# Performance work log

Hardware: AMD Instinct MI355X
Metric: run time of the kernel (lower is better)

Reference implementation:

```python
import jax, jax.numpy as jnp
import numpy as np

B, L, INPUT_DIM = 4, 4096, 32
D_MODEL, N_LAYERS = 256, 2
D_STATE, D_CONV, EXPAND = 16, 4, 2
D_INNER = EXPAND * D_MODEL          # 512
DT_RANK = (D_MODEL + 15) // 16      # 16
OUTPUT_DIM, HORIZON = 32, 4
LN_EPS = 1e-5


def setup_inputs() -> dict:
    key = jax.random.key(0)
    ks = jax.random.split(key, 16)
    s = 0.02
    inp = {
        "x": jax.random.normal(ks[0], (B, L, INPUT_DIM), jnp.float32),
        "enc_w": jax.random.normal(ks[1], (D_MODEL, INPUT_DIM), jnp.float32) * s,
        "enc_b": jnp.zeros((D_MODEL,), jnp.float32),
        "in_proj_w": jax.random.normal(ks[2], (N_LAYERS, 2 * D_INNER, D_MODEL), jnp.float32) * s,
        "conv_w": jax.random.normal(ks[3], (N_LAYERS, D_INNER, D_CONV), jnp.float32) * s,
        "conv_b": jnp.zeros((N_LAYERS, D_INNER), jnp.float32),
        "xproj_w": jax.random.normal(ks[4], (N_LAYERS, DT_RANK + 2 * D_STATE, D_INNER), jnp.float32) * s,
        "dtproj_w": jax.random.normal(ks[5], (N_LAYERS, D_INNER, DT_RANK), jnp.float32) * s,
        "dtproj_b": jax.random.normal(ks[6], (N_LAYERS, D_INNER), jnp.float32) * 0.1,
        "A_log": jnp.log(jnp.tile(jnp.arange(1.0, D_STATE + 1.0, dtype=jnp.float32), (N_LAYERS, D_INNER, 1))),
        "Dp": jnp.ones((N_LAYERS, D_INNER), jnp.float32),
        "out_proj_w": jax.random.normal(ks[7], (N_LAYERS, D_MODEL, D_INNER), jnp.float32) * s,
        "ln_g": jnp.ones((D_MODEL,), jnp.float32),
        "ln_b": jnp.zeros((D_MODEL,), jnp.float32),
        "head_w": jax.random.normal(ks[8], (OUTPUT_DIM * HORIZON, D_MODEL), jnp.float32) * s,
        "head_b": jnp.zeros((OUTPUT_DIM * HORIZON,), jnp.float32),
    }
    return inp


def _mamba_block(x, in_w, cw, cb, xp_w, dt_w, dt_b, A_log, Dp, out_w):
    # x: [B, L, d_model]
    b, l, _ = x.shape
    xz = jnp.einsum("bld,ed->ble", x, in_w)            # [B, L, 2*d_inner]
    xi, res = jnp.split(xz, 2, axis=-1)
    # causal depthwise conv1d (padding=d_conv-1, truncated to L)
    xpad = jnp.pad(xi, ((0, 0), (D_CONV - 1, 0), (0, 0)))
    xi = sum(xpad[:, k:k + l, :] * cw[:, k] for k in range(D_CONV)) + cb
    xi = jax.nn.silu(xi)
    dbl = jnp.einsum("bld,ed->ble", xi, xp_w)           # [B, L, dt_rank+2*d_state]
    dt = dbl[..., :DT_RANK]
    Bm = dbl[..., DT_RANK:DT_RANK + D_STATE]            # [B, L, d_state]
    Cm = dbl[..., DT_RANK + D_STATE:]                   # [B, L, d_state]
    dt = jax.nn.softplus(jnp.einsum("blr,dr->bld", dt, dt_w) + dt_b)  # [B, L, d_inner]
    A = -jnp.exp(A_log)                                 # [d_inner, d_state]

    def step(h, ins):
        dt_t, B_t, C_t, x_t = ins                       # [B,di],[B,ds],[B,ds],[B,di]
        dA = jnp.exp(dt_t[..., None] * A)               # [B, d_inner, d_state]
        h = dA * h + (dt_t * x_t)[..., None] * B_t[:, None, :]
        y = jnp.einsum("bds,bs->bd", h, C_t)
        return h, y

    h0 = jnp.zeros((b, D_INNER, D_STATE), x.dtype)
    xs = (jnp.moveaxis(dt, 1, 0), jnp.moveaxis(Bm, 1, 0),
          jnp.moveaxis(Cm, 1, 0), jnp.moveaxis(xi, 1, 0))
    _, ys = jax.lax.scan(step, h0, xs)                  # ys: [L, B, d_inner]
    y = jnp.moveaxis(ys, 0, 1) + xi * Dp
    y = y * jax.nn.silu(res)
    return jnp.einsum("ble,de->bld", y, out_w)


def reference(x, enc_w, enc_b, in_proj_w, conv_w, conv_b, xproj_w, dtproj_w,
              dtproj_b, A_log, Dp, out_proj_w, ln_g, ln_b, head_w, head_b):
    h = jnp.einsum("bli,di->bld", x, enc_w) + enc_b     # encoder
    for i in range(N_LAYERS):
        h = h + _mamba_block(h, in_proj_w[i], conv_w[i], conv_b[i], xproj_w[i],
                             dtproj_w[i], dtproj_b[i], A_log[i], Dp[i], out_proj_w[i])
    mu = jnp.mean(h, axis=-1, keepdims=True)
    var = jnp.mean((h - mu) ** 2, axis=-1, keepdims=True)
    hn = (h - mu) * jax.lax.rsqrt(var + LN_EPS) * ln_g + ln_b
    state = hn[:, -1, :]                                # last timestep
    return jnp.einsum("bd,od->bo", state, head_w) + head_b
```

## Files before the change

### kernel.cpp

```cpp
#include <hip/hip_runtime.h>
#include <hip/hip_bf16.h>
#include <math.h>

#define BB 4
#define LL 4096
#define DM 256
#define DI 512
#define DS 16
#define NOUTK 128
#define LN_EPS 1e-5f
#define NC 128
#define CLEN (LL/NC)
#define BL (BB*LL)
#define LDB 640

typedef __attribute__((ext_vector_type(8))) short short8;
typedef __attribute__((ext_vector_type(4))) float f32x4;

__device__ __forceinline__ ushort f2bf(float f) {
    union { float f; unsigned u; } v; v.f = f;
    unsigned r = (v.u + 0x7FFF + ((v.u >> 16) & 1)) >> 16;
    return (ushort)r;
}
__device__ __forceinline__ float bf2f(ushort u) {
    union { unsigned u; float f; } v; v.u = ((unsigned)u) << 16;
    return v.f;
}

__global__ __launch_bounds__(256) void cast_bf16_kernel(
    const float* __restrict__ src, ushort* __restrict__ dst, int n)
{
    int i = blockIdx.x * 256 + threadIdx.x;
    if (i < n) dst[i] = f2bf(src[i]);
}

__global__ __launch_bounds__(256) void build_comb_kernel(
    const float* __restrict__ xpw, const float* __restrict__ dtw,
    ushort* __restrict__ dst)
{
    int i = blockIdx.x * 256 + threadIdx.x;
    int l = i / (640 * 512);
    int rem = i - l * 640 * 512;
    int row = rem >> 9, k = rem & 511;
    const float* xp = xpw + l * 48 * 512;
    const float* dw = dtw + l * 512 * 16;
    float v;
    if (row < 512) {
        v = 0.f;
        #pragma unroll
        for (int r = 0; r < 16; ++r)
            v = fmaf(dw[row * 16 + r], xp[r * 512 + k], v);
    } else if (row < 544) {
        v = xp[(row - 512 + 16) * 512 + k];
    } else v = 0.f;
    dst[i] = f2bf(v);
}

__global__ __launch_bounds__(256) void enc_kernel(
    const float* __restrict__ x, const float* __restrict__ w,
    const float* __restrict__ b, float* __restrict__ h,
    ushort* __restrict__ hbf)
{
    __shared__ float sw[256 * 33];
    __shared__ float sx[4][32];
    int tid = threadIdx.x;
    for (int i = tid; i < 256 * 8; i += 256) {
        float4 v = ((const float4*)w)[i];
        int r = i >> 3, c = (i & 7) * 4;
        sw[r * 33 + c + 0] = v.x; sw[r * 33 + c + 1] = v.y;
        sw[r * 33 + c + 2] = v.z; sw[r * 33 + c + 3] = v.w;
    }
    int row0 = blockIdx.x * 4;
    if (tid < 32) {
        for (int rr = 0; rr < 4; ++rr)
            sx[rr][tid] = x[(size_t)(row0 + rr) * 32 + tid];
    }
    __syncthreads();
    float bb = b[tid];
    #pragma unroll
    for (int rr = 0; rr < 4; ++rr) {
        float acc = bb;
        #pragma unroll
        for (int k = 0; k < 32; ++k)
            acc = fmaf(sx[rr][k], sw[tid * 33 + k], acc);
        size_t o = (size_t)(row0 + rr) * DM + tid;
        h[o] = acc;
        hbf[o] = f2bf(acc);
    }
}

template<int EPI, bool F32OUT, bool RESID, bool BF16OUT>
__global__ __launch_bounds__(256, 4) void mfma_gemm(
    const ushort* __restrict__ A, int lda,
    const ushort* __restrict__ W,
    const float* __restrict__ bias,
    float* __restrict__ C, int ldc,
    ushort* __restrict__ Cbf, int ldcbf,
    int K)
{
    __shared__ ushort As[64 * 64];
    __shared__ ushort Ws[128 * 64];
    const int tid = threadIdx.x;

    int nwg = gridDim.x * gridDim.y;
    int wlin = blockIdx.y * gridDim.x + blockIdx.x;
    int gx = blockIdx.x, gy = blockIdx.y;
    if ((nwg & 7) == 0) {
        int q = nwg >> 3;
        int s = (wlin & 7) * q + (wlin >> 3);
        gx = s % gridDim.x;
        gy = s / gridDim.x;
    }
    const int bm = gy * 64;
    const int bn = gx * 128;
    const int wid = tid >> 6, lane = tid & 63;
    const int wrow = (wid >> 1) * 32, wcol = (wid & 1) * 64;
    const int sr = tid >> 3;
    const int sc = tid & 7;

    f32x4 acc[2][4];
    #pragma unroll
    for (int mi = 0; mi < 2; ++mi)
        #pragma unroll
        for (int ni = 0; ni < 4; ++ni)
            acc[mi][ni] = (f32x4){0.f, 0.f, 0.f, 0.f};

    const int nk = K >> 6;
    for (int t = 0; t < nk; ++t) {
        const int k0 = t << 6;
        #pragma unroll
        for (int it = 0; it < 2; ++it) {
            int r = it * 32 + sr;
            int csrc = sc ^ (r & 7);
            __builtin_amdgcn_global_load_lds(
                (const __attribute__((address_space(1))) unsigned int*)
                    (A + (size_t)(bm + r) * lda + k0 + csrc * 8),
                (__attribute__((address_space(3))) unsigned int*)
                    (As + r * 64 + sc * 8), 16, 0, 0);
        }
        #pragma unroll
        for (int it = 0; it < 4; ++it) {
            int r = it * 32 + sr;
            int csrc = sc ^ (r & 7);
            __builtin_amdgcn_global_load_lds(
                (const __attribute__((address_space(1))) unsigned int*)
                    (W + (size_t)(bn + r) * K + k0 + csrc * 8),
                (__attribute__((address_space(3))) unsigned int*)
                    (Ws + r * 64 + sc * 8), 16, 0, 0);
        }
        __syncthreads();
        #pragma unroll
        for (int kk = 0; kk < 2; ++kk) {
            short8 af[2], bfr[4];
            #pragma unroll
            for (int mi = 0; mi < 2; ++mi) {
                int r = wrow + mi * 16 + (lane & 15);
                int c = (lane >> 4) + kk * 4;
                af[mi] = *(const short8*)(As + r * 64 + ((c ^ (r & 7)) << 3));
            }
            #pragma unroll
            for (int ni = 0; ni < 4; ++ni) {
                int r = wcol + ni * 16 + (lane & 15);
                int c = (lane >> 4) + kk * 4;
                bfr[ni] = *(const short8*)(Ws + r * 64 + ((c ^ (r & 7)) << 3));
            }
            #pragma unroll
            for (int mi = 0; mi < 2; ++mi)
                #pragma unroll
                for (int ni = 0; ni < 4; ++ni)
                    acc[mi][ni] = __builtin_amdgcn_mfma_f32_16x16x32_bf16(
                        af[mi], bfr[ni], acc[mi][ni], 0, 0, 0);
        }
        __syncthreads();
    }

    #pragma unroll
    for (int mi = 0; mi < 2; ++mi)
        #pragma unroll
        for (int ni = 0; ni < 4; ++ni) {
            int col = bn + wcol + ni * 16 + (lane & 15);
            #pragma unroll
            for (int r = 0; r < 4; ++r) {
                int row = bm + wrow + mi * 16 + (lane >> 4) * 4 + r;
                float v = acc[mi][ni][r];
                if (EPI == 1) {
                    if (col < 512) {
                        float u = v + bias[col];
                        float sp = fmaxf(u, 0.f) + __logf(1.f + __expf(-fabsf(u)));
                        Cbf[(size_t)row * ldcbf + col] = f2bf(sp);
                    } else if (col < 544) {
                        C[(size_t)row * ldc + (col - 512)] = v;
                    }
                } else {
                    if (F32OUT) {
                        float* cp = C + (size_t)row * ldc + col;
                        float vv = v;
                        if (RESID) vv += *cp;
                        *cp = vv;
                        if (BF16OUT) Cbf[(size_t)row * ldcbf + col] = f2bf(vv);
                    } else if (BF16OUT) {
                        Cbf[(size_t)row * ldcbf + col] = f2bf(v);
                    }
                }
            }
        }
}

__global__ __launch_bounds__(256) void conv_silu_kernel(
    const ushort* __restrict__ xz, const float* __restrict__ cw,
    const float* __restrict__ cb, ushort* __restrict__ xi)
{
    int idx = blockIdx.x * 256 + threadIdx.x;
    int d4 = (idx & 127) * 4;
    int bt = idx >> 7;
    int t = bt & (LL - 1);
    const ushort* base = xz + (size_t)bt * 1024 + d4;
    float acc[4];
    float4 w[4];
    #pragma unroll
    for (int j = 0; j < 4; ++j) {
        acc[j] = cb[d4 + j];
        w[j] = *(const float4*)(cw + (d4 + j) * 4);
    }
    #pragma unroll
    for (int k = 0; k < 4; ++k) {
        int back = 3 - k;
        if (t >= back) {
            ushort4 v = *(const ushort4*)(base - back * 1024);
            float wk0 = (k==0)?w[0].x:(k==1)?w[0].y:(k==2)?w[0].z:w[0].w;
            float wk1 = (k==0)?w[1].x:(k==1)?w[1].y:(k==2)?w[1].z:w[1].w;
            float wk2 = (k==0)?w[2].x:(k==1)?w[2].y:(k==2)?w[2].z:w[2].w;
            float wk3 = (k==0)?w[3].x:(k==1)?w[3].y:(k==2)?w[3].z:w[3].w;
            acc[0] = fmaf(bf2f(v.x), wk0, acc[0]);
            acc[1] = fmaf(bf2f(v.y), wk1, acc[1]);
            acc[2] = fmaf(bf2f(v.z), wk2, acc[2]);
            acc[3] = fmaf(bf2f(v.w), wk3, acc[3]);
        }
    }
    ushort4 o;
    float s0 = acc[0] / (1.f + __expf(-acc[0]));
    float s1 = acc[1] / (1.f + __expf(-acc[1]));
    float s2 = acc[2] / (1.f + __expf(-acc[2]));
    float s3 = acc[3] / (1.f + __expf(-acc[3]));
    o.x = f2bf(s0); o.y = f2bf(s1); o.z = f2bf(s2); o.w = f2bf(s3);
    *(ushort4*)(xi + (size_t)bt * 512 + d4) = o;
}

__global__ __launch_bounds__(256) void scan_phase1(
    const ushort* __restrict__ xi, const ushort* __restrict__ dtb,
    const float* __restrict__ bc,
    const float* __restrict__ alog,
    float* __restrict__ cA, float* __restrict__ cH)
{
    int d = blockIdx.z * 256 + threadIdx.x;
    int b = blockIdx.y, c = blockIdx.x;
    float Av[16];
    bool fast = true;
    #pragma unroll
    for (int s = 0; s < 16; ++s) {
        Av[s] = -__expf(alog[d * 16 + s]);
        fast = fast && (fabsf(Av[s] + (float)(s + 1)) < 1e-3f * (s + 1));
    }
    float h[16], P[16];
    #pragma unroll
    for (int s = 0; s < 16; ++s) { h[s] = 0.f; P[s] = 1.f; }
    int t0 = c * CLEN;
    if (fast) {
        float Pe = 1.f;
        for (int t = t0; t < t0 + CLEN; ++t) {
            size_t row = (size_t)b * LL + t;
            float dt = bf2f(dtb[row * 512 + d]);
            float x = bf2f(xi[row * 512 + d]);
            float dtx = dt * x;
            const float* bp = bc + row * 32;
            float e1 = __expf(-dt);
            float e2=e1*e1, e3=e2*e1, e4=e2*e2, e5=e3*e2, e6=e3*e3, e7=e4*e3, e8=e4*e4;
            float e9=e5*e4, e10=e5*e5, e11=e6*e5, e12=e6*e6, e13=e7*e6, e14=e7*e7, e15=e8*e7, e16=e8*e8;
            float pw[16] = {e1,e2,e3,e4,e5,e6,e7,e8,e9,e10,e11,e12,e13,e14,e15,e16};
            #pragma unroll
            for (int s = 0; s < 16; ++s)
                h[s] = fmaf(pw[s], h[s], dtx * bp[s]);
            Pe *= e1;
        }
        float p1=Pe, p2=p1*p1, p3=p2*p1, p4=p2*p2, p5=p3*p2, p6=p3*p3, p7=p4*p3, p8=p4*p4;
        float p9=p5*p4, p10=p5*p5, p11=p6*p5, p12=p6*p6, p13=p7*p6, p14=p7*p7, p15=p8*p7, p16=p8*p8;
        float pp[16] = {p1,p2,p3,p4,p5,p6,p7,p8,p9,p10,p11,p12,p13,p14,p15,p16};
        #pragma unroll
        for (int s = 0; s < 16; ++s) P[s] = pp[s];
    } else {
        for (int t = t0; t < t0 + CLEN; ++t) {
            size_t row = (size_t)b * LL + t;
            float dt = bf2f(dtb[row * 512 + d]);
            float x = bf2f(xi[row * 512 + d]);
            float dtx = dt * x;
            const float* bp = bc + row * 32;
            #pragma unroll
            for (int s = 0; s < 16; ++s) {
                float dA = __expf(dt * Av[s]);
                h[s] = fmaf(dA, h[s], dtx * bp[s]);
                P[s] *= dA;
            }
        }
    }
    size_t base = (((size_t)b * DI + d) * NC + c) * 16;
    #pragma unroll
    for (int q = 0; q < 4; ++q) {
        *(float4*)(cA + base + q*4) = *(float4*)&P[q*4];
        *(float4*)(cH + base + q*4) = *(float4*)&h[q*4];
    }
}

__global__ __launch_bounds__(256) void scan_phase2(
    const float* __restrict__ cA, float* __restrict__ cH)
{
    int idx = blockIdx.x * 256 + threadIdx.x;
    int s = idx & 15;
    int bd = idx >> 4;
    size_t base = (size_t)bd * NC * 16 + s;
    float init = 0.f;
    for (int c = 0; c < NC; ++c) {
        size_t o = base + (size_t)c * 16;
        float a = cA[o], hh = cH[o];
        cH[o] = init;
        init = fmaf(a, init, hh);
    }
}

__global__ __launch_bounds__(256) void scan_phase3(
    const ushort* __restrict__ xz,
    ushort* __restrict__ xi,
    const ushort* __restrict__ dtb,
    const float* __restrict__ bc,
    const float* __restrict__ alog,
    const float* __restrict__ Dp,
    const float* __restrict__ cH,
    int c0)
{
    int d = blockIdx.z * 256 + threadIdx.x;
    int b = blockIdx.y;
    int c = blockIdx.x + c0;
    float Av[16];
    bool fast = true;
    #pragma unroll
    for (int s = 0; s < 16; ++s) {
        Av[s] = -__expf(alog[d * 16 + s]);
        fast = fast && (fabsf(Av[s] + (float)(s + 1)) < 1e-3f * (s + 1));
    }
    float h[16];
    size_t cbase = (((size_t)b * DI + d) * NC + c) * 16;
    #pragma unroll
    for (int q = 0; q < 4; ++q)
        *(float4*)&h[q*4] = *(const float4*)(cH + cbase + q*4);
    float Dd = Dp[d];
    int t0 = c * CLEN;
    if (fast) {
        for (int t = t0; t < t0 + CLEN; ++t) {
            size_t row = (size_t)b * LL + t;
            float dt = bf2f(dtb[row * 512 + d]);
            float x = bf2f(xi[row * 512 + d]);
            float dtx = dt * x;
            const float* bp = bc + row * 32;
            const float* cp = bc + row * 32 + 16;
            float e1 = __expf(-dt);
            float e2=e1*e1, e3=e2*e1, e4=e2*e2, e5=e3*e2, e6=e3*e3, e7=e4*e3, e8=e4*e4;
            float e9=e5*e4, e10=e5*e5, e11=e6*e5, e12=e6*e6, e13=e7*e6, e14=e7*e7, e15=e8*e7, e16=e8*e8;
            float pw[16] = {e1,e2,e3,e4,e5,e6,e7,e8,e9,e10,e11,e12,e13,e14,e15,e16};
            float y = 0.f;
            #pragma unroll
            for (int s = 0; s < 16; ++s) {
                h[s] = fmaf(pw[s], h[s], dtx * bp[s]);
                y = fmaf(h[s], cp[s], y);
            }
            float res = bf2f(xz[row * 1024 + 512 + d]);
            float g = (y + x * Dd) * (res / (1.f + __expf(-res)));
            xi[row * 512 + d] = f2bf(g);
        }
    } else {
        for (int t = t0; t < t0 + CLEN; ++t) {
            size_t row = (size_t)b * LL + t;
            float dt = bf2f(dtb[row * 512 + d]);
            float x = bf2f(xi[row * 512 + d]);
            float dtx = dt * x;
            const float* bp = bc + row * 32;
            const float* cp = bc + row * 32 + 16;
            float y = 0.f;
            #pragma unroll
            for (int s = 0; s < 16; ++s) {
                float dA = __expf(dt * Av[s]);
                h[s] = fmaf(dA, h[s], dtx * bp[s]);
                y = fmaf(h[s], cp[s], y);
            }
            float res = bf2f(xz[row * 1024 + 512 + d]);
            float g = (y + x * Dd) * (res / (1.f + __expf(-res)));
            xi[row * 512 + d] = f2bf(g);
        }
    }
}

__global__ __launch_bounds__(256) void out_proj_last_kernel(
    const ushort* __restrict__ xi, const float* __restrict__ W,
    float* __restrict__ h)
{
    int b = blockIdx.x, n = threadIdx.x;
    __shared__ float sy[DI];
    const ushort* yrow = xi + ((size_t)b * LL + (LL - 1)) * DI;
    for (int k = threadIdx.x; k < DI; k += 256) sy[k] = bf2f(yrow[k]);
    __syncthreads();
    const float* wr = W + (size_t)n * DI;
    float acc = 0.f;
    for (int k = 0; k < DI; k += 4) {
        float4 wv = *(const float4*)(wr + k);
        acc = fmaf(sy[k+0], wv.x, acc);
        acc = fmaf(sy[k+1], wv.y, acc);
        acc = fmaf(sy[k+2], wv.z, acc);
        acc = fmaf(sy[k+3], wv.w, acc);
    }
    h[((size_t)b * LL + (LL - 1)) * DM + n] += acc;
}

__global__ __launch_bounds__(256) void ln_head_kernel(
    const float* __restrict__ h, const float* __restrict__ lng,
    const float* __restrict__ lnb, const float* __restrict__ hw,
    const float* __restrict__ hb, float* __restrict__ out)
{
    int b = blockIdx.x, tid = threadIdx.x;
    __shared__ float sh[DM];
    __shared__ float r1[4], r2[4];
    float v = h[((size_t)b * LL + (LL - 1)) * DM + tid];
    float s = v;
    #pragma unroll
    for (int o = 32; o >= 1; o >>= 1) s += __shfl_down(s, o);
    if ((tid & 63) == 0) r1[tid >> 6] = s;
    __syncthreads();
    float mu = (r1[0] + r1[1] + r1[2] + r1[3]) * (1.f / 256.f);
    float dv = v - mu;
    float q = dv * dv;
    #pragma unroll
    for (int o = 32; o >= 1; o >>= 1) q += __shfl_down(q, o);
    if ((tid & 63) == 0) r2[tid >> 6] = q;
    __syncthreads();
    float var = (r2[0] + r2[1] + r2[2] + r2[3]) * (1.f / 256.f);
    sh[tid] = dv * rsqrtf(var + LN_EPS) * lng[tid] + lnb[tid];
    __syncthreads();
    if (tid < NOUTK) {
        const float* wr = hw + (size_t)tid * DM;
        float acc = hb[tid];
        for (int d2 = 0; d2 < DM; d2 += 4) {
            float4 wv = *(const float4*)(wr + d2);
            acc = fmaf(sh[d2+0], wv.x, acc);
            acc = fmaf(sh[d2+1], wv.y, acc);
            acc = fmaf(sh[d2+2], wv.z, acc);
            acc = fmaf(sh[d2+3], wv.w, acc);
        }
        out[b * NOUTK + tid] = acc;
    }
}

extern "C" void kernel_launch(void* const* d_in, const int* in_sizes, int n_in,
                              void* d_out, int out_size, void* d_ws, size_t ws_size,
                              hipStream_t stream)
{
    const float* x    = (const float*)d_in[0];
    const float* encw = (const float*)d_in[1];
    const float* encb = (const float*)d_in[2];
    const float* inw  = (const float*)d_in[3];
    const float* cw   = (const float*)d_in[4];
    const float* cb   = (const float*)d_in[5];
    const float* xpw  = (const float*)d_in[6];
    const float* dtw  = (const float*)d_in[7];
    const float* dtb  = (const float*)d_in[8];
    const float* alog = (const float*)d_in[9];
    const float* Dp   = (const float*)d_in[10];
    const float* opw  = (const float*)d_in[11];
    const float* lng  = (const float*)d_in[12];
    const float* lnb  = (const float*)d_in[13];
    const float* hw   = (const float*)d_in[14];
    const float* hb   = (const float*)d_in[15];
    float* out = (float*)d_out;

    float* ws   = (float*)d_ws;
    float* h    = ws;
    float* bc   = h   + (size_t)BL * DM;
    float* cA   = bc  + (size_t)BL * 32;
    float* cH   = cA  + (size_t)BB * DI * NC * DS;
    ushort* h_bf    = (ushort*)(cH + (size_t)BB * DI * NC * DS);
    ushort* xz_bf   = h_bf  + (size_t)BL * DM;
    ushort* xi_bf   = xz_bf + (size_t)BL * 1024;
    ushort* dt_bf   = xi_bf + (size_t)BL * DI;
    ushort* inw_bf  = dt_bf + (size_t)BL * DI;
    ushort* opw_bf  = inw_bf + 2 * 1024 * DM;
    ushort* comb_bf = opw_bf + 2 * DM * DI;

    dim3 blk(256, 1, 1);

    cast_bf16_kernel<<<dim3((2*1024*DM)/256), blk, 0, stream>>>(inw, inw_bf, 2*1024*DM);
    cast_bf16_kernel<<<dim3((2*DM*DI)/256), blk, 0, stream>>>(opw, opw_bf, 2*DM*DI);
    build_comb_kernel<<<dim3((2*640*512)/256), blk, 0, stream>>>(xpw, dtw, comb_bf);

    enc_kernel<<<dim3(BL/4), blk, 0, stream>>>(x, encw, encb, h, h_bf);

    for (int l = 0; l < 2; ++l) {
        mfma_gemm<0,false,false,true><<<dim3(1024/128, BL/64), blk, 0, stream>>>(
            h_bf, DM, inw_bf + (size_t)l * 1024 * DM, nullptr,
            nullptr, 0, xz_bf, 1024, DM);
        conv_silu_kernel<<<dim3(BL * 128 / 256), blk, 0, stream>>>(
            xz_bf, cw + l * DI * 4, cb + l * DI, xi_bf);
        mfma_gemm<1,false,false,false><<<dim3(LDB/128, BL/64), blk, 0, stream>>>(
            xi_bf, DI, comb_bf + (size_t)l * LDB * DI, dtb + l * DI,
            bc, 32, dt_bf, 512, DI);
        scan_phase1<<<dim3(NC, BB, 2), blk, 0, stream>>>(
            xi_bf, dt_bf, bc, alog + (size_t)l * DI * 16, cA, cH);
        scan_phase2<<<dim3(BB * DI * DS / 256), blk, 0, stream>>>(cA, cH);
        if (l == 0) {
            scan_phase3<<<dim3(NC, BB, 2), blk, 0, stream>>>(
                xz_bf, xi_bf, dt_bf, bc, alog + (size_t)l * DI * 16,
                Dp + l * DI, cH, 0);
            mfma_gemm<0,true,true,true><<<dim3(DM/128, BL/64), blk, 0, stream>>>(
                xi_bf, DI, opw_bf + (size_t)l * DM * DI, nullptr,
                h, DM, h_bf, DM, DI);
        } else {
            scan_phase3<<<dim3(1, BB, 2), blk, 0, stream>>>(
                xz_bf, xi_bf, dt_bf, bc, alog + (size_t)l * DI * 16,
                Dp + l * DI, cH, NC - 1);
            out_proj_last_kernel<<<dim3(BB), blk, 0, stream>>>(
                xi_bf, opw + (size_t)l * DM * DI, h);
        }
    }

    ln_head_kernel<<<dim3(BB), blk, 0, stream>>>(h, lng, lnb, hw, hb, out);
}
```

Measured before the change: 344.0 us.

## Parallelize chunk-carry scan with warp-shuffle prefix across chunks

Replaces the serial 128-step loop over chunks in scan_phase2 with a parallel scan: each (b,d) pair gets a block, with 16 lanes per state each handling 8 chunks, combined by a shuffle-based prefix over 16 lanes. This cuts the long dependent chain of global loads per thread and launches more threads. It adds shuffle overhead and a strided memory access pattern.

Result: slower. 369.7 us (+7.5%).

```diff
diff --git a/kernel.cpp b/kernel.cpp
--- a/kernel.cpp
+++ b/kernel.cpp
@@ -313,16 +313,36 @@
 __global__ __launch_bounds__(256) void scan_phase2(
     const float* __restrict__ cA, float* __restrict__ cH)
 {
-    int idx = blockIdx.x * 256 + threadIdx.x;
-    int s = idx & 15;
-    int bd = idx >> 4;
+    int bd = blockIdx.x;
+    int tid = threadIdx.x;
+    int s = tid >> 4;
+    int g = tid & 15;
     size_t base = (size_t)bd * NC * 16 + s;
-    float init = 0.f;
-    for (int c = 0; c < NC; ++c) {
-        size_t o = base + (size_t)c * 16;
-        float a = cA[o], hh = cH[o];
+    float a8[8], h8[8];
+    #pragma unroll
+    for (int j = 0; j < 8; ++j) {
+        size_t o = base + (size_t)(g * 8 + j) * 16;
+        a8[j] = cA[o]; h8[j] = cH[o];
+    }
+    float A = 1.f, H = 0.f;
+    #pragma unroll
+    for (int j = 0; j < 8; ++j) {
+        H = fmaf(a8[j], H, h8[j]);
+        A *= a8[j];
+    }
+    #pragma unroll
+    for (int off = 1; off < 16; off <<= 1) {
+        float Ap = __shfl_up(A, off, 16);
+        float Hp = __shfl_up(H, off, 16);
+        if (g >= off) { H = fmaf(A, Hp, H); A *= Ap; }
+    }
+    float init = __shfl_up(H, 1, 16);
+    if (g == 0) init = 0.f;
+    #pragma unroll
+    for (int j = 0; j < 8; ++j) {
+        size_t o = base + (size_t)(g * 8 + j) * 16;
         cH[o] = init;
-        init = fmaf(a, init, hh);
+        init = fmaf(a8[j], init, h8[j]);
     }
 }
 
@@ -510,7 +530,7 @@
             bc, 32, dt_bf, 512, DI);
         scan_phase1<<<dim3(NC, BB, 2), blk, 0, stream>>>(
             xi_bf, dt_bf, bc, alog + (size_t)l * DI * 16, cA, cH);
-        scan_phase2<<<dim3(BB * DI * DS / 256), blk, 0, stream>>>(cA, cH);
+        scan_phase2<<<dim3(BB * DI), blk, 0, stream>>>(cA, cH);
         if (l == 0) {
             scan_phase3<<<dim3(NC, BB, 2), blk, 0, stream>>>(
                 xz_bf, xi_bf, dt_bf, bc, alog + (size_t)l * DI * 16,
```
